# Kernel optimization log

Hardware: AMD Instinct MI355X
Metric: run time of the kernel (lower is better)

The kernel has to match this reference:

```python
import jax, jax.numpy as jnp
import numpy as np

N_NODES = 50000
N_EDGES = 800000
SD = 128
N_GRAPHS = 128
HL = 4
VOCAB = 1340
N_CLASSES = 41
BN_EPS = 1e-5


def setup_inputs() -> dict:
    key = jax.random.key(0)
    ks = jax.random.split(key, 20)
    s = 1.0 / np.sqrt(SD)
    inp = {
        "node_ids": jax.random.randint(ks[0], (N_NODES,), 0, VOCAB),
        "edge_index": jax.random.randint(ks[1], (2, N_EDGES), 0, N_NODES),
        "batch": jnp.sort(jax.random.randint(ks[2], (N_NODES,), 0, N_GRAPHS)),
        "emb": jax.random.normal(ks[3], (VOCAB, SD)) * 0.05,
        "in_W1": jax.random.normal(ks[4], (SD, SD)) * s,
        "in_b1": jnp.zeros((SD,)),
        "in_W2": jax.random.normal(ks[5], (SD, SD)) * s,
        "in_b2": jnp.zeros((SD,)),
        "bn_gamma": jnp.ones((SD,)),
        "bn_beta": jnp.zeros((SD,)),
        "bn_mean": jnp.zeros((SD,)),
        "bn_var": jnp.ones((SD,)),
        "out_W1": jax.random.normal(ks[6], (SD, SD)) * s,
        "out_b1": jnp.zeros((SD,)),
        "out_W2": jax.random.normal(ks[7], (SD, SD)) * s,
        "out_b2": jnp.zeros((SD,)),
        "fc1_W": jax.random.normal(ks[8], (SD, SD)) * s,
        "fc1_b": jnp.zeros((SD,)),
        "fc2_W": jax.random.normal(ks[9], (N_CLASSES, SD)) * s,
        "fc2_b": jnp.zeros((N_CLASSES,)),
    }
    return inp


def reference(node_ids, edge_index, batch, emb, in_W1, in_b1, in_W2, in_b2,
              bn_gamma, bn_beta, bn_mean, bn_var,
              out_W1, out_b1, out_W2, out_b2, fc1_W, fc1_b, fc2_W, fc2_b):
    src, dst = edge_index[0], edge_index[1]

    def gin(x, W1, b1, W2, b2):
        # GINConv with eps=0: mlp(x + sum_{j in N(i)} x_j)
        agg = jax.ops.segment_sum(x[src], dst, num_segments=N_NODES)
        h = x + agg
        h = jnp.maximum(h @ W1.T + b1, 0.0)
        return h @ W2.T + b2

    def bn(x):
        # eval-mode BatchNorm1d with running stats
        return (x - bn_mean) * (bn_gamma / jnp.sqrt(bn_var + BN_EPS)) + bn_beta

    x = emb[node_ids]  # [N, SD]
    x = bn(jnp.maximum(gin(x, in_W1, in_b1, in_W2, in_b2), 0.0))
    for _ in range(HL):  # shared weights, repeated hl times
        x = bn(jnp.maximum(gin(x, in_W1, in_b1, in_W2, in_b2), 0.0))
    x = jnp.maximum(gin(x, out_W1, out_b1, out_W2, out_b2), 0.0)
    pooled = jax.ops.segment_sum(x, batch, num_segments=N_GRAPHS)  # [G, SD]
    h = jnp.maximum(pooled @ fc1_W.T + fc1_b, 0.0)
    return h @ fc2_W.T + fc2_b  # [G, 41]
```

## Files before the change

kernel.cpp:

```cpp
#include <hip/hip_runtime.h>

#define NN 50000
#define NE 800000
#define NG 128
#define NC 41
#define CAP 64

typedef __attribute__((ext_vector_type(8))) short bfrag8;
typedef __attribute__((ext_vector_type(4))) float facc4;

__device__ __forceinline__ float bf2f(unsigned short u) {
  union { unsigned int i; float f; } v; v.i = ((unsigned int)u) << 16; return v.f;
}
__device__ __forceinline__ unsigned short f2bf(float f) {
  union { float f; unsigned int i; } v; v.f = f;
  unsigned int x = v.i;
  x += 0x7fffu + ((x >> 16) & 1u);
  return (unsigned short)(x >> 16);
}
__device__ __forceinline__ void acc_u4(const uint4 u, float* a) {
  union { unsigned int i; float f; } c;
  c.i = u.x << 16;          a[0] += c.f;
  c.i = u.x & 0xffff0000u;  a[1] += c.f;
  c.i = u.y << 16;          a[2] += c.f;
  c.i = u.y & 0xffff0000u;  a[3] += c.f;
  c.i = u.z << 16;          a[4] += c.f;
  c.i = u.z & 0xffff0000u;  a[5] += c.f;
  c.i = u.w << 16;          a[6] += c.f;
  c.i = u.w & 0xffff0000u;  a[7] += c.f;
}
__device__ __forceinline__ unsigned int pack2(float lo, float hi) {
  return (unsigned int)f2bf(lo) | ((unsigned int)f2bf(hi) << 16);
}

__global__ void prep_kernel(const float* __restrict__ W1, const float* __restrict__ W2,
                            const float* __restrict__ oW1, const float* __restrict__ oW2,
                            const float* __restrict__ gamma, const float* __restrict__ beta,
                            const float* __restrict__ mean, const float* __restrict__ var,
                            unsigned short* W1b, unsigned short* W2b,
                            unsigned short* oW1b, unsigned short* oW2b,
                            float* scale, float* shift) {
  int i = blockIdx.x * 256 + threadIdx.x;
  if (i < 128 * 128) {
    W1b[i] = f2bf(W1[i]);
    W2b[i] = f2bf(W2[i]);
    oW1b[i] = f2bf(oW1[i]);
    oW2b[i] = f2bf(oW2[i]);
  }
  if (i < 128) {
    float s = gamma[i] * rsqrtf(var[i] + 1e-5f);
    scale[i] = s;
    shift[i] = beta[i] - mean[i] * s;
  }
}

__global__ void embed_kernel(const int* __restrict__ node_ids, const float* __restrict__ emb,
                             unsigned short* __restrict__ xb) {
  int idx = blockIdx.x * 256 + threadIdx.x;
  if (idx >= NN * 32) return;
  int node = idx >> 5, f = (idx & 31) * 4;
  const float4 v = *(const float4*)&emb[node_ids[node] * 128 + f];
  ushort4 o;
  o.x = f2bf(v.x); o.y = f2bf(v.y); o.z = f2bf(v.z); o.w = f2bf(v.w);
  *(ushort4*)&xb[node * 128 + f] = o;
}

__global__ void fill_kernel(const int* __restrict__ ei, int* __restrict__ cnt,
                            int* __restrict__ srclist) {
  int e = blockIdx.x * 256 + threadIdx.x;
  if (e >= NE) return;
  int s = ei[e];
  int d = ei[NE + e];
  int pos = atomicAdd(&cnt[d], 1);
  if (pos < CAP) srclist[d * CAP + pos] = s;
}

__global__ __launch_bounds__(256) void agg_kernel(const unsigned short* __restrict__ xb,
                                                  const int* __restrict__ cnt,
                                                  const int* __restrict__ srclist,
                                                  unsigned short* __restrict__ hb) {
  int tid = threadIdx.x;
  int node = blockIdx.x * 16 + (tid >> 4);
  if (node >= NN) return;
  int f = (tid & 15) * 8;
  float a[8];
  acc_u4(*(const uint4*)&xb[node * 128 + f],
         (a[0]=0.f, a[1]=0.f, a[2]=0.f, a[3]=0.f, a[4]=0.f, a[5]=0.f, a[6]=0.f, a[7]=0.f, a));
  int deg = cnt[node];
  if (deg > CAP) deg = CAP;
  const int* lst = &srclist[node * CAP];
  int j = 0;
  for (; j + 8 <= deg; j += 8) {
    uint4 u0 = *(const uint4*)&xb[lst[j] * 128 + f];
    uint4 u1 = *(const uint4*)&xb[lst[j + 1] * 128 + f];
    uint4 u2 = *(const uint4*)&xb[lst[j + 2] * 128 + f];
    uint4 u3 = *(const uint4*)&xb[lst[j + 3] * 128 + f];
    uint4 u4 = *(const uint4*)&xb[lst[j + 4] * 128 + f];
    uint4 u5 = *(const uint4*)&xb[lst[j + 5] * 128 + f];
    uint4 u6 = *(const uint4*)&xb[lst[j + 6] * 128 + f];
    uint4 u7 = *(const uint4*)&xb[lst[j + 7] * 128 + f];
    acc_u4(u0, a); acc_u4(u1, a); acc_u4(u2, a); acc_u4(u3, a);
    acc_u4(u4, a); acc_u4(u5, a); acc_u4(u6, a); acc_u4(u7, a);
  }
  for (; j + 4 <= deg; j += 4) {
    uint4 u0 = *(const uint4*)&xb[lst[j] * 128 + f];
    uint4 u1 = *(const uint4*)&xb[lst[j + 1] * 128 + f];
    uint4 u2 = *(const uint4*)&xb[lst[j + 2] * 128 + f];
    uint4 u3 = *(const uint4*)&xb[lst[j + 3] * 128 + f];
    acc_u4(u0, a); acc_u4(u1, a); acc_u4(u2, a); acc_u4(u3, a);
  }
  for (; j < deg; ++j) {
    uint4 u = *(const uint4*)&xb[lst[j] * 128 + f];
    acc_u4(u, a);
  }
  uint4 o;
  o.x = pack2(a[0], a[1]); o.y = pack2(a[2], a[3]);
  o.z = pack2(a[4], a[5]); o.w = pack2(a[6], a[7]);
  *(uint4*)&hb[node * 128 + f] = o;
}

__global__ __launch_bounds__(256) void mlp_kernel(const unsigned short* __restrict__ A,
                                                  const unsigned short* __restrict__ W1b,
                                                  const unsigned short* __restrict__ W2b,
                                                  const float* __restrict__ bias1,
                                                  const float* __restrict__ bias2,
                                                  const float* __restrict__ scale,
                                                  const float* __restrict__ shift,
                                                  unsigned short* __restrict__ Out,
                                                  int M, int mode) {
  __shared__ unsigned short sW1[128 * 128];
  __shared__ unsigned short sW2[128 * 128];
  __shared__ unsigned short sA[64 * 128];
  int tid = threadIdx.x;
  int bRow = blockIdx.x * 64;

  const uint4* gw1 = (const uint4*)W1b;
  const uint4* gw2 = (const uint4*)W2b;
#pragma unroll
  for (int p = 0; p < 8; ++p) {
    int g = p * 256 + tid;
    int r = g >> 4, b = g & 15;
    int ph = (b + r) & 15;
    *(uint4*)&sW1[(r * 16 + ph) * 8] = gw1[g];
    *(uint4*)&sW2[(r * 16 + ph) * 8] = gw2[g];
  }
#pragma unroll
  for (int p = 0; p < 4; ++p) {
    int g = p * 256 + tid;
    int r = g >> 4, b = g & 15;
    int ph = (b + r) & 15;
    int grow = bRow + r;
    uint4 v = {0u, 0u, 0u, 0u};
    if (grow < M) v = *(const uint4*)&A[grow * 128 + b * 8];
    *(uint4*)&sA[(r * 16 + ph) * 8] = v;
  }
  __syncthreads();

  int wave = tid >> 6;
  int lane = tid & 63;
  int l16 = lane & 15;
  int quad = lane >> 4;
  int arow = wave * 16 + l16;

  {
    bfrag8 af[4];
#pragma unroll
    for (int k = 0; k < 4; ++k) {
      int ph = (k * 4 + quad + arow) & 15;
      af[k] = *(const bfrag8*)&sA[(arow * 16 + ph) * 8];
    }
    facc4 acc[8];
#pragma unroll
    for (int t = 0; t < 8; ++t) acc[t] = (facc4){0.f, 0.f, 0.f, 0.f};
#pragma unroll
    for (int k = 0; k < 4; ++k) {
#pragma unroll
      for (int t = 0; t < 8; ++t) {
        int r = t * 16 + l16;
        int ph = (k * 4 + quad + r) & 15;
        bfrag8 bf = *(const bfrag8*)&sW1[(r * 16 + ph) * 8];
        acc[t] = __builtin_amdgcn_mfma_f32_16x16x32_bf16(af[k], bf, acc[t], 0, 0, 0);
      }
    }
#pragma unroll
    for (int t = 0; t < 8; ++t) {
      int col = t * 16 + l16;
      float b = bias1[col];
      int cb = col >> 3, ce = col & 7;
#pragma unroll
      for (int i = 0; i < 4; ++i) {
        int row = wave * 16 + quad * 4 + i;
        float v = acc[t][i] + b;
        int ph = (cb + row) & 15;
        sA[(row * 16 + ph) * 8 + ce] = f2bf(v > 0.f ? v : 0.f);
      }
    }
  }

  {
    bfrag8 af[4];
#pragma unroll
    for (int k = 0; k < 4; ++k) {
      int ph = (k * 4 + quad + arow) & 15;
      af[k] = *(const bfrag8*)&sA[(arow * 16 + ph) * 8];
    }
    facc4 acc[8];
#pragma unroll
    for (int t = 0; t < 8; ++t) acc[t] = (facc4){0.f, 0.f, 0.f, 0.f};
#pragma unroll
    for (int k = 0; k < 4; ++k) {
#pragma unroll
      for (int t = 0; t < 8; ++t) {
        int r = t * 16 + l16;
        int ph = (k * 4 + quad + r) & 15;
        bfrag8 bf = *(const bfrag8*)&sW2[(r * 16 + ph) * 8];
        acc[t] = __builtin_amdgcn_mfma_f32_16x16x32_bf16(af[k], bf, acc[t], 0, 0, 0);
      }
    }
#pragma unroll
    for (int t = 0; t < 8; ++t) {
      int col = t * 16 + l16;
      float b = bias2[col];
      float sc = 1.f, sh = 0.f;
      if (mode == 1) { sc = scale[col]; sh = shift[col]; }
      int cb = col >> 3, ce = col & 7;
#pragma unroll
      for (int i = 0; i < 4; ++i) {
        int row = wave * 16 + quad * 4 + i;
        float v = acc[t][i] + b;
        v = v > 0.f ? v : 0.f;
        if (mode == 1) v = v * sc + sh;
        int ph = (cb + row) & 15;
        sA[(row * 16 + ph) * 8 + ce] = f2bf(v);
      }
    }
  }
  __syncthreads();

#pragma unroll
  for (int p = 0; p < 4; ++p) {
    int g = p * 256 + tid;
    int r = g >> 4, b = g & 15;
    int ph = (b + r) & 15;
    int grow = bRow + r;
    if (grow < M)
      *(uint4*)&Out[grow * 128 + b * 8] = *(const uint4*)&sA[(r * 16 + ph) * 8];
  }
}

__global__ __launch_bounds__(128) void pool_kernel(const unsigned short* __restrict__ xb,
                                                   const int* __restrict__ batch,
                                                   float* __restrict__ pooled) {
  const int CHUNK = 128;
  int start = blockIdx.x * CHUNK;
  int end = start + CHUNK;
  if (end > NN) end = NN;
  int f = threadIdx.x;
  float acc = 0.f;
  int cur = -1;
  for (int i = start; i < end; ++i) {
    int b = batch[i];
    if (b != cur) {
      if (cur >= 0) atomicAdd(&pooled[cur * 128 + f], acc);
      cur = b;
      acc = 0.f;
    }
    acc += bf2f(xb[i * 128 + f]);
  }
  if (cur >= 0) atomicAdd(&pooled[cur * 128 + f], acc);
}

__global__ void fc1_kernel(const float* __restrict__ pooled, const float* __restrict__ W,
                           const float* __restrict__ b, float* __restrict__ out) {
  int idx = blockIdx.x * 256 + threadIdx.x;
  if (idx >= NG * 128) return;
  int r = idx >> 7, c = idx & 127;
  float acc = 0.f;
  for (int k = 0; k < 128; ++k) acc += pooled[r * 128 + k] * W[c * 128 + k];
  acc += b[c];
  out[idx] = acc > 0.f ? acc : 0.f;
}

__global__ void fc2_kernel(const float* __restrict__ h1, const float* __restrict__ W,
                           const float* __restrict__ b, float* __restrict__ out) {
  int idx = blockIdx.x * 256 + threadIdx.x;
  if (idx >= NG * NC) return;
  int r = idx / NC, c = idx % NC;
  float acc = 0.f;
  for (int k = 0; k < 128; ++k) acc += h1[r * 128 + k] * W[c * 128 + k];
  out[idx] = acc + b[c];
}

extern "C" void kernel_launch(void* const* d_in, const int* in_sizes, int n_in,
                              void* d_out, int out_size, void* d_ws, size_t ws_size,
                              hipStream_t stream) {
  const int* node_ids = (const int*)d_in[0];
  const int* edge_index = (const int*)d_in[1];
  const int* batch = (const int*)d_in[2];
  const float* emb = (const float*)d_in[3];
  const float* in_W1 = (const float*)d_in[4];
  const float* in_b1 = (const float*)d_in[5];
  const float* in_W2 = (const float*)d_in[6];
  const float* in_b2 = (const float*)d_in[7];
  const float* bn_gamma = (const float*)d_in[8];
  const float* bn_beta = (const float*)d_in[9];
  const float* bn_mean = (const float*)d_in[10];
  const float* bn_var = (const float*)d_in[11];
  const float* out_W1 = (const float*)d_in[12];
  const float* out_b1 = (const float*)d_in[13];
  const float* out_W2 = (const float*)d_in[14];
  const float* out_b2 = (const float*)d_in[15];
  const float* fc1_W = (const float*)d_in[16];
  const float* fc1_b = (const float*)d_in[17];
  const float* fc2_W = (const float*)d_in[18];
  const float* fc2_b = (const float*)d_in[19];
  float* out = (float*)d_out;

  char* ws = (char*)d_ws;
  size_t off = 0;
  auto alloc = [&](size_t bytes) {
    char* p = ws + off;
    off = (off + bytes + 255) & ~(size_t)255;
    return p;
  };
  unsigned short* xb = (unsigned short*)alloc((size_t)NN * 128 * 2);
  unsigned short* hb = (unsigned short*)alloc((size_t)NN * 128 * 2);
  int* srclist = (int*)alloc((size_t)NN * CAP * 4);
  int* cnt = (int*)alloc((size_t)NN * 4);
  unsigned short* W1b = (unsigned short*)alloc(128 * 128 * 2);
  unsigned short* W2b = (unsigned short*)alloc(128 * 128 * 2);
  unsigned short* oW1b = (unsigned short*)alloc(128 * 128 * 2);
  unsigned short* oW2b = (unsigned short*)alloc(128 * 128 * 2);
  float* bnscale = (float*)alloc(128 * 4);
  float* bnshift = (float*)alloc(128 * 4);
  float* pooled = (float*)alloc(NG * 128 * 4);
  float* h1 = (float*)alloc(NG * 128 * 4);

  hipMemsetAsync(cnt, 0, (size_t)NN * 4, stream);
  hipMemsetAsync(pooled, 0, (size_t)NG * 128 * 4, stream);

  prep_kernel<<<64, 256, 0, stream>>>(in_W1, in_W2, out_W1, out_W2,
                                      bn_gamma, bn_beta, bn_mean, bn_var,
                                      W1b, W2b, oW1b, oW2b, bnscale, bnshift);
  fill_kernel<<<(NE + 255) / 256, 256, 0, stream>>>(edge_index, cnt, srclist);
  embed_kernel<<<(NN * 32 + 255) / 256, 256, 0, stream>>>(node_ids, emb, xb);

  int mlp_blocks = (NN + 63) / 64;
  for (int l = 0; l < 6; ++l) {
    const unsigned short* w1 = (l < 5) ? W1b : oW1b;
    const unsigned short* w2 = (l < 5) ? W2b : oW2b;
    const float* b1 = (l < 5) ? in_b1 : out_b1;
    const float* b2 = (l < 5) ? in_b2 : out_b2;
    int mode2 = (l < 5) ? 1 : 0;
    agg_kernel<<<(NN + 15) / 16, 256, 0, stream>>>(xb, cnt, srclist, hb);
    mlp_kernel<<<mlp_blocks, 256, 0, stream>>>(hb, w1, w2, b1, b2, bnscale, bnshift,
                                               xb, NN, mode2);
  }

  pool_kernel<<<(NN + 127) / 128, 128, 0, stream>>>(xb, batch, pooled);
  fc1_kernel<<<(NG * 128 + 255) / 256, 256, 0, stream>>>(pooled, fc1_W, fc1_b, h1);
  fc2_kernel<<<(NG * NC + 255) / 256, 256, 0, stream>>>(h1, fc2_W, fc2_b, out);
}
```

Baseline: 502.7 us.

## Split each node's neighbor gather across four wave slots with shuffle reduction

The aggregation kernel now gives each node a full 64-lane wave instead of 16 lanes. Four slots of 16 lanes each take interleaved neighbors and gather them, and the partial sums are combined with cross-lane xor shuffles before slot 0 writes the result. The goal is more memory-level parallelism per node and less serial latency from long neighbor lists, since the average degree is about 16. The cost is four times as many threads and blocks, shuffle overhead, and lanes left idle on low-degree nodes.

```diff
diff --git a/kernel.cpp b/kernel.cpp
--- a/kernel.cpp
+++ b/kernel.cpp
@@ -80,43 +80,58 @@
                                                   const int* __restrict__ srclist,
                                                   unsigned short* __restrict__ hb) {
   int tid = threadIdx.x;
-  int node = blockIdx.x * 16 + (tid >> 4);
+  int wave = tid >> 6;
+  int lane = tid & 63;
+  int node = blockIdx.x * 4 + wave;
   if (node >= NN) return;
-  int f = (tid & 15) * 8;
+  int slot = lane >> 4;
+  int chunk = lane & 15;
+  int f = chunk * 8;
+
   float a[8];
-  acc_u4(*(const uint4*)&xb[node * 128 + f],
-         (a[0]=0.f, a[1]=0.f, a[2]=0.f, a[3]=0.f, a[4]=0.f, a[5]=0.f, a[6]=0.f, a[7]=0.f, a));
+#pragma unroll
+  for (int i = 0; i < 8; ++i) a[i] = 0.f;
+  if (slot == 0) acc_u4(*(const uint4*)&xb[node * 128 + f], a);
+
   int deg = cnt[node];
   if (deg > CAP) deg = CAP;
   const int* lst = &srclist[node * CAP];
-  int j = 0;
-  for (; j + 8 <= deg; j += 8) {
-    uint4 u0 = *(const uint4*)&xb[lst[j] * 128 + f];
-    uint4 u1 = *(const uint4*)&xb[lst[j + 1] * 128 + f];
-    uint4 u2 = *(const uint4*)&xb[lst[j + 2] * 128 + f];
-    uint4 u3 = *(const uint4*)&xb[lst[j + 3] * 128 + f];
-    uint4 u4 = *(const uint4*)&xb[lst[j + 4] * 128 + f];
-    uint4 u5 = *(const uint4*)&xb[lst[j + 5] * 128 + f];
-    uint4 u6 = *(const uint4*)&xb[lst[j + 6] * 128 + f];
-    uint4 u7 = *(const uint4*)&xb[lst[j + 7] * 128 + f];
+
+  int j = slot;
+  for (; j + 12 < deg; j += 16) {
+    int n0 = lst[j];
+    int n1 = lst[j + 4];
+    int n2 = lst[j + 8];
+    int n3 = lst[j + 12];
+    uint4 u0 = *(const uint4*)&xb[n0 * 128 + f];
+    uint4 u1 = *(const uint4*)&xb[n1 * 128 + f];
+    uint4 u2 = *(const uint4*)&xb[n2 * 128 + f];
+    uint4 u3 = *(const uint4*)&xb[n3 * 128 + f];
     acc_u4(u0, a); acc_u4(u1, a); acc_u4(u2, a); acc_u4(u3, a);
-    acc_u4(u4, a); acc_u4(u5, a); acc_u4(u6, a); acc_u4(u7, a);
-  }
-  for (; j + 4 <= deg; j += 4) {
-    uint4 u0 = *(const uint4*)&xb[lst[j] * 128 + f];
-    uint4 u1 = *(const uint4*)&xb[lst[j + 1] * 128 + f];
-    uint4 u2 = *(const uint4*)&xb[lst[j + 2] * 128 + f];
-    uint4 u3 = *(const uint4*)&xb[lst[j + 3] * 128 + f];
-    acc_u4(u0, a); acc_u4(u1, a); acc_u4(u2, a); acc_u4(u3, a);
-  }
-  for (; j < deg; ++j) {
+  }
+  for (; j + 4 < deg; j += 8) {
+    int n0 = lst[j];
+    int n1 = lst[j + 4];
+    uint4 u0 = *(const uint4*)&xb[n0 * 128 + f];
+    uint4 u1 = *(const uint4*)&xb[n1 * 128 + f];
+    acc_u4(u0, a); acc_u4(u1, a);
+  }
+  if (j < deg) {
     uint4 u = *(const uint4*)&xb[lst[j] * 128 + f];
     acc_u4(u, a);
   }
-  uint4 o;
-  o.x = pack2(a[0], a[1]); o.y = pack2(a[2], a[3]);
-  o.z = pack2(a[4], a[5]); o.w = pack2(a[6], a[7]);
-  *(uint4*)&hb[node * 128 + f] = o;
+
+#pragma unroll
+  for (int i = 0; i < 8; ++i) {
+    a[i] += __shfl_xor(a[i], 16, 64);
+    a[i] += __shfl_xor(a[i], 32, 64);
+  }
+  if (slot == 0) {
+    uint4 o;
+    o.x = pack2(a[0], a[1]); o.y = pack2(a[2], a[3]);
+    o.z = pack2(a[4], a[5]); o.w = pack2(a[6], a[7]);
+    *(uint4*)&hb[node * 128 + f] = o;
+  }
 }
 
 __global__ __launch_bounds__(256) void mlp_kernel(const unsigned short* __restrict__ A,
@@ -352,7 +367,7 @@
     const float* b1 = (l < 5) ? in_b1 : out_b1;
     const float* b2 = (l < 5) ? in_b2 : out_b2;
     int mode2 = (l < 5) ? 1 : 0;
-    agg_kernel<<<(NN + 15) / 16, 256, 0, stream>>>(xb, cnt, srclist, hb);
+    agg_kernel<<<(NN + 3) / 4, 256, 0, stream>>>(xb, cnt, srclist, hb);
     mlp_kernel<<<mlp_blocks, 256, 0, stream>>>(hb, w1, w2, b1, b2, bnscale, bnshift,
                                                xb, NN, mode2);
   }
```

New measurement: 507.8 us. About the same (+1.0%).
